# Kernel optimization log

Measured on AMD Instinct MI355X. Metric: run time of the kernel, lower is better.

Reference implementation:

```python
import jax, jax.numpy as jnp
import numpy as np

N = 100000   # num_nodes
D = 64       # input_dim
H = 128      # 2 * input_dim
E = 1_600_000
EPS = 1e-5   # BatchNorm1d eps


def setup_inputs() -> dict:
    key = jax.random.key(0)
    ks = jax.random.split(key, 8)
    # Embedding: xavier_normal_, padding_idx=0 row zeroed
    emb = jax.random.normal(ks[0], (N, D), jnp.float32) * np.float32(np.sqrt(2.0 / (N + D)))
    emb = emb.at[0].set(0.0)
    # GCNConv weights (glorot-ish scaling)
    W1 = jax.random.normal(ks[1], (D, H), jnp.float32) * np.float32(np.sqrt(2.0 / (D + H)))
    b1 = jnp.zeros((H,), jnp.float32)
    W2 = jax.random.normal(ks[2], (H, D), jnp.float32) * np.float32(np.sqrt(2.0 / (H + D)))
    b2 = jnp.zeros((D,), jnp.float32)
    gamma = jnp.ones((D,), jnp.float32)
    beta = jnp.zeros((D,), jnp.float32)
    edge_index = jax.random.randint(ks[3], (2, E), 0, N, dtype=jnp.int64)
    return {"emb": emb, "W1": W1, "b1": b1, "W2": W2, "b2": b2,
            "gamma": gamma, "beta": beta, "edge_index": edge_index}


def reference(emb, W1, b1, W2, b2, gamma, beta, edge_index):
    # --- gcn_norm: add self-loops, symmetric normalization (PyG default) ---
    self_loops = jnp.arange(N, dtype=edge_index.dtype)
    row = jnp.concatenate([edge_index[0], self_loops])  # source j
    col = jnp.concatenate([edge_index[1], self_loops])  # target i
    deg = jax.ops.segment_sum(jnp.ones(row.shape[0], emb.dtype), col, num_segments=N)
    deg_inv_sqrt = jnp.where(deg > 0, jax.lax.rsqrt(jnp.maximum(deg, 1.0)), 0.0)
    norm = deg_inv_sqrt[row] * deg_inv_sqrt[col]  # [E+N]

    def gcn_conv(x, W, b):
        h = x @ W                                  # linear first (PyG GCNConv)
        msg = h[row] * norm[:, None]               # gather + normalize
        out = jax.ops.segment_sum(msg, col, num_segments=N)  # scatter-aggregate
        return out + b

    h = gcn_conv(emb, W1, b1)   # [N, H]
    # dropout: identity in eval mode (deterministic reference)
    h = gcn_conv(h, W2, b2)     # [N, D]

    # BatchNorm1d, training-mode batch statistics (biased variance)
    mean = h.mean(axis=0)
    var = h.var(axis=0)
    return (h - mean) * jax.lax.rsqrt(var + EPS) * gamma + beta
```

## Files before the change

### kernel.cpp

```cpp
#include <hip/hip_runtime.h>


#define EPS_BN 1e-5f
#define NBKT_PAD 1024
#define BN_NB 128
#define SCAT_B 256

typedef _Float16 f16;
typedef _Float16 f16x2 __attribute__((ext_vector_type(2)));
typedef _Float16 f16x8 __attribute__((ext_vector_type(8)));
typedef float f32x4 __attribute__((ext_vector_type(4)));
union pk4 { ushort4 u; f16 h[4]; f16x2 h2[2]; };

__global__ __launch_bounds__(1024) void hist_k(const int* __restrict__ colv, int E, int epb,
                                               int* __restrict__ ghist) {
    __shared__ int bins[NBKT_PAD];
    int tid = threadIdx.x;
    bins[tid] = 0;
    __syncthreads();
    int e0 = blockIdx.x * epb;
    int e1 = min(E, e0 + epb);
    for (int e = e0 + tid; e < e1; e += 1024)
        atomicAdd(&bins[colv[e] >> 7], 1);
    __syncthreads();
    ghist[blockIdx.x * NBKT_PAD + tid] = bins[tid];
}

__global__ __launch_bounds__(256) void scan_bucket_k(int* __restrict__ ghist, int* __restrict__ bcnt) {
    __shared__ int s[256];
    int k = blockIdx.x;
    int b = threadIdx.x;
    int v = ghist[b * NBKT_PAD + k];
    s[b] = v; __syncthreads();
    for (int off = 1; off < 256; off <<= 1) {
        int t = (b >= off) ? s[b - off] : 0;
        __syncthreads();
        s[b] += t;
        __syncthreads();
    }
    ghist[b * NBKT_PAD + k] = s[b] - v;
    if (b == 255) bcnt[k] = s[255];
}

__global__ __launch_bounds__(1024) void scan_total_k(const int* __restrict__ bcnt,
                                                     int* __restrict__ bstart,
                                                     int* __restrict__ start, int n, int E) {
    __shared__ int s[1024];
    int tid = threadIdx.x;
    int v = bcnt[tid];
    s[tid] = v; __syncthreads();
    for (int off = 1; off < 1024; off <<= 1) {
        int t = (tid >= off) ? s[tid - off] : 0;
        __syncthreads();
        s[tid] += t;
        __syncthreads();
    }
    bstart[tid] = s[tid] - v;
    if (tid == 1023) bstart[1024] = s[1023];
    if (tid == 0) start[n] = E;
}

__global__ __launch_bounds__(1024) void scatB_k(const int* __restrict__ rowv, const int* __restrict__ colv,
                                                int E, int epb, const int* __restrict__ ghist,
                                                const int* __restrict__ bstart,
                                                unsigned* __restrict__ ebuf) {
    __shared__ int bins[NBKT_PAD];
    int tid = threadIdx.x;
    bins[tid] = ghist[blockIdx.x * NBKT_PAD + tid] + bstart[tid];
    __syncthreads();
    int e0 = blockIdx.x * epb;
    int e1 = min(E, e0 + epb);
    for (int e = e0 + tid; e < e1; e += 1024) {
        int c = colv[e];
        int p = atomicAdd(&bins[c >> 7], 1);
        ebuf[p] = ((unsigned)rowv[e] << 7) | (unsigned)(c & 127);
    }
}

__global__ __launch_bounds__(512) void buildC_k(const unsigned* __restrict__ ebuf,
                                                const int* __restrict__ bstart,
                                                int* __restrict__ start, int* __restrict__ srcs,
                                                float* __restrict__ dis, int n) {
    __shared__ int ncnt[128], noff[128], stmp[128];
    int b = blockIdx.x;
    int tid = threadIdx.x;
    int e0 = bstart[b], e1 = bstart[b + 1];
    if (tid < 128) ncnt[tid] = 0;
    __syncthreads();
    for (int e = e0 + tid; e < e1; e += 512)
        atomicAdd(&ncnt[ebuf[e] & 127u], 1);
    __syncthreads();
    if (tid < 128) stmp[tid] = ncnt[tid];
    __syncthreads();
    for (int off = 1; off < 128; off <<= 1) {
        int t = (tid < 128 && tid >= off) ? stmp[tid - off] : 0;
        __syncthreads();
        if (tid < 128) stmp[tid] += t;
        __syncthreads();
    }
    if (tid < 128) {
        int excl = stmp[tid] - ncnt[tid];
        noff[tid] = e0 + excl;
        int node = b * 128 + tid;
        if (node < n) {
            start[node] = e0 + excl;
            dis[node] = rsqrtf((float)(ncnt[tid] + 1));
        }
    }
    __syncthreads();
    for (int e = e0 + tid; e < e1; e += 512) {
        unsigned p = ebuf[e];
        int pos = atomicAdd(&noff[p & 127u], 1);
        srcs[pos] = (int)(p >> 7);
    }
}

__global__ __launch_bounds__(256) void wprep_k(const float* __restrict__ W1, const float* __restrict__ W2,
                                               f16* __restrict__ w1t, f16* __restrict__ w2t) {
    int t = blockIdx.x * 256 + threadIdx.x;
    if (t < 8192) {
        int k = t >> 7, c = t & 127;
        w1t[c * 64 + k] = (f16)W1[t];
    } else if (t < 16384) {
        int i = t - 8192;
        int k = i >> 6, c = i & 63;
        w2t[c * 128 + k] = (f16)W2[i];
    }
}

__global__ __launch_bounds__(256) void prescale_k(const float* __restrict__ emb,
                                                  const float* __restrict__ dis,
                                                  f16* __restrict__ es, int n) {
    int gid = blockIdx.x * 256 + threadIdx.x;
    int node = gid >> 4, q = gid & 15;
    if (node >= n) return;
    float d = dis[node];
    float4 v = ((const float4*)emb)[(size_t)node * 16 + q];
    pk4 p;
    p.h[0] = (f16)(v.x * d); p.h[1] = (f16)(v.y * d);
    p.h[2] = (f16)(v.z * d); p.h[3] = (f16)(v.w * d);
    ((ushort4*)es)[(size_t)node * 16 + q] = p.u;
}

__device__ __forceinline__ void acc_pk(float4& acc, ushort4 u) {
    pk4 p; p.u = u;
    acc.x += (float)p.h[0]; acc.y += (float)p.h[1];
    acc.z += (float)p.h[2]; acc.w += (float)p.h[3];
}

__global__ __launch_bounds__(256) void agg64_k(const f16* __restrict__ table, const int* __restrict__ start,
                                               const int* __restrict__ srcs, const float* __restrict__ dis,
                                               const float* __restrict__ bias, f16* __restrict__ out, int n) {
    int node = blockIdx.x * 16 + (threadIdx.x >> 4);
    if (node >= n) return;
    int lane = threadIdx.x & 15;
    const ushort4* t4 = (const ushort4*)table;
    float4 acc = make_float4(0.f, 0.f, 0.f, 0.f);
    acc_pk(acc, t4[(size_t)node * 16 + lane]);
    int s0 = start[node], s1 = start[node + 1];
    int e = s0;
    for (; e + 7 < s1; e += 8) {
        int i0 = srcs[e],     i1 = srcs[e + 1], i2 = srcs[e + 2], i3 = srcs[e + 3];
        int i4 = srcs[e + 4], i5 = srcs[e + 5], i6 = srcs[e + 6], i7 = srcs[e + 7];
        ushort4 v0 = t4[(size_t)i0 * 16 + lane];
        ushort4 v1 = t4[(size_t)i1 * 16 + lane];
        ushort4 v2 = t4[(size_t)i2 * 16 + lane];
        ushort4 v3 = t4[(size_t)i3 * 16 + lane];
        ushort4 v4 = t4[(size_t)i4 * 16 + lane];
        ushort4 v5 = t4[(size_t)i5 * 16 + lane];
        ushort4 v6 = t4[(size_t)i6 * 16 + lane];
        ushort4 v7 = t4[(size_t)i7 * 16 + lane];
        acc_pk(acc, v0); acc_pk(acc, v1); acc_pk(acc, v2); acc_pk(acc, v3);
        acc_pk(acc, v4); acc_pk(acc, v5); acc_pk(acc, v6); acc_pk(acc, v7);
    }
    for (; e + 3 < s1; e += 4) {
        int i0 = srcs[e], i1 = srcs[e + 1], i2 = srcs[e + 2], i3 = srcs[e + 3];
        ushort4 v0 = t4[(size_t)i0 * 16 + lane];
        ushort4 v1 = t4[(size_t)i1 * 16 + lane];
        ushort4 v2 = t4[(size_t)i2 * 16 + lane];
        ushort4 v3 = t4[(size_t)i3 * 16 + lane];
        acc_pk(acc, v0); acc_pk(acc, v1); acc_pk(acc, v2); acc_pk(acc, v3);
    }
    for (; e < s1; e++) acc_pk(acc, t4[(size_t)srcs[e] * 16 + lane]);
    float d = dis[node];
    float4 b = make_float4(0.f, 0.f, 0.f, 0.f);
    if (bias) b = ((const float4*)bias)[lane];
    pk4 p;
    p.h[0] = (f16)(acc.x * d + b.x); p.h[1] = (f16)(acc.y * d + b.y);
    p.h[2] = (f16)(acc.z * d + b.z); p.h[3] = (f16)(acc.w * d + b.w);
    ((ushort4*)out)[(size_t)node * 16 + lane] = p.u;
}

#define SH_PAD 136
__global__ __launch_bounds__(256) void gemmAB_mfma_k(const f16* __restrict__ ag1,
                                                     const f16* __restrict__ w1t,
                                                     const float* __restrict__ b1,
                                                     const f16* __restrict__ w2t,
                                                     const float* __restrict__ dis,
                                                     f16* __restrict__ hs2, int n) {
    __shared__ f16 sH[64 * SH_PAD];
    int tid = threadIdx.x;
    int w = tid >> 6, l = tid & 63;
    int cl = l & 15, ko = (l >> 4) * 8, r0 = (l >> 4) * 4;
    int rowbase = blockIdx.x * 64;
    int mrow = rowbase + w * 16;

    f16x8 a0 = *(const f16x8*)(ag1 + (size_t)(mrow + cl) * 64 + ko);
    f16x8 a1 = *(const f16x8*)(ag1 + (size_t)(mrow + cl) * 64 + 32 + ko);
#pragma unroll
    for (int nt = 0; nt < 8; nt++) {
        f32x4 acc = {0.f, 0.f, 0.f, 0.f};
        f16x8 b0 = *(const f16x8*)(w1t + (nt * 16 + cl) * 64 + ko);
        f16x8 b1f = *(const f16x8*)(w1t + (nt * 16 + cl) * 64 + 32 + ko);
        acc = __builtin_amdgcn_mfma_f32_16x16x32_f16(a0, b0, acc, 0, 0, 0);
        acc = __builtin_amdgcn_mfma_f32_16x16x32_f16(a1, b1f, acc, 0, 0, 0);
        float bias = b1[nt * 16 + cl];
#pragma unroll
        for (int j = 0; j < 4; j++)
            sH[(w * 16 + r0 + j) * SH_PAD + nt * 16 + cl] = (f16)(acc[j] + bias);
    }
    __syncthreads();
#pragma unroll
    for (int nt = 0; nt < 4; nt++) {
        f32x4 acc = {0.f, 0.f, 0.f, 0.f};
#pragma unroll
        for (int s = 0; s < 4; s++) {
            f16x8 a = *(const f16x8*)(&sH[(w * 16 + cl) * SH_PAD + s * 32 + ko]);
            f16x8 b = *(const f16x8*)(w2t + (nt * 16 + cl) * 128 + s * 32 + ko);
            acc = __builtin_amdgcn_mfma_f32_16x16x32_f16(a, b, acc, 0, 0, 0);
        }
#pragma unroll
        for (int j = 0; j < 4; j++) {
            int row = mrow + r0 + j;
            if (row < n) {
                float d = dis[row];
                hs2[(size_t)row * 64 + nt * 16 + cl] = (f16)(acc[j] * d);
            }
        }
    }
}

__global__ __launch_bounds__(256) void bn_part_k(const f16* __restrict__ x, float* __restrict__ pbuf, int n) {
    __shared__ float4 ls[256], lq[256];
    int q = threadIdx.x & 15;
    int rg = threadIdx.x >> 4;
    float4 s = make_float4(0.f, 0.f, 0.f, 0.f);
    float4 ss = make_float4(0.f, 0.f, 0.f, 0.f);
    for (int row = blockIdx.x * 16 + rg; row < n; row += gridDim.x * 16) {
        pk4 p; p.u = ((const ushort4*)x)[(size_t)row * 16 + q];
        float v0 = p.h[0], v1 = p.h[1], v2 = p.h[2], v3 = p.h[3];
        s.x += v0; s.y += v1; s.z += v2; s.w += v3;
        ss.x += v0 * v0; ss.y += v1 * v1; ss.z += v2 * v2; ss.w += v3 * v3;
    }
    ls[threadIdx.x] = s; lq[threadIdx.x] = ss;
    __syncthreads();
    if (threadIdx.x < 16) {
        float4 S = make_float4(0.f, 0.f, 0.f, 0.f);
        float4 Q = make_float4(0.f, 0.f, 0.f, 0.f);
        for (int g = 0; g < 16; g++) {
            float4 a = ls[g * 16 + threadIdx.x], b = lq[g * 16 + threadIdx.x];
            S.x += a.x; S.y += a.y; S.z += a.z; S.w += a.w;
            Q.x += b.x; Q.y += b.y; Q.z += b.z; Q.w += b.w;
        }
        float4* dst = (float4*)(pbuf + (size_t)blockIdx.x * 128);
        dst[threadIdx.x] = S;
        dst[threadIdx.x + 16] = Q;
    }
}

__global__ __launch_bounds__(64) void bn_final_k(const float* __restrict__ pbuf,
                                                 const float* __restrict__ gamma, const float* __restrict__ beta,
                                                 int n, float* __restrict__ scale, float* __restrict__ shift) {
    int c = threadIdx.x;
    float s = 0.f, q = 0.f;
    for (int b = 0; b < BN_NB; b++) {
        s += pbuf[b * 128 + c];
        q += pbuf[b * 128 + 64 + c];
    }
    float inv_n = 1.f / (float)n;
    float mean = s * inv_n;
    float var = q * inv_n - mean * mean;
    float sc = gamma[c] * rsqrtf(var + EPS_BN);
    scale[c] = sc;
    shift[c] = beta[c] - mean * sc;
}

__global__ __launch_bounds__(256) void bn_apply_k(const f16* __restrict__ x, const float* __restrict__ scale,
                                                  const float* __restrict__ shift, float* __restrict__ out, int n) {
    __shared__ float sscale[64], sshift[64];
    if (threadIdx.x < 64) {
        sscale[threadIdx.x] = scale[threadIdx.x];
        sshift[threadIdx.x] = shift[threadIdx.x];
    }
    __syncthreads();
    int i = blockIdx.x * 256 + threadIdx.x;
    if (i < n * 16) {
        int c = (i & 15) * 4;
        pk4 p; p.u = ((const ushort4*)x)[i];
        float4 o;
        o.x = (float)p.h[0] * sscale[c]     + sshift[c];
        o.y = (float)p.h[1] * sscale[c + 1] + sshift[c + 1];
        o.z = (float)p.h[2] * sscale[c + 2] + sshift[c + 2];
        o.w = (float)p.h[3] * sscale[c + 3] + sshift[c + 3];
        ((float4*)out)[i] = o;
    }
}

extern "C" void kernel_launch(void* const* d_in, const int* in_sizes, int n_in,
                              void* d_out, int out_size, void* d_ws, size_t ws_size,
                              hipStream_t stream) {
    const float* emb   = (const float*)d_in[0];
    const float* W1    = (const float*)d_in[1];
    const float* b1    = (const float*)d_in[2];
    const float* W2    = (const float*)d_in[3];
    const float* b2    = (const float*)d_in[4];
    const float* gamma = (const float*)d_in[5];
    const float* beta  = (const float*)d_in[6];
    const int*   ei    = (const int*)d_in[7];
    const int n = in_sizes[0] / 64;
    const int E = in_sizes[7] / 2;
    const int* rowv = ei;
    const int* colv = ei + E;
    const int NBKT = (n + 127) / 128;

    char* ws = (char*)d_ws;
    size_t o = 0;
    auto alloc = [&](size_t bytes) -> char* {
        char* p = ws + o;
        o = (o + bytes + 255) & ~(size_t)255;
        return p;
    };
    int*   ghist   = (int*)alloc((size_t)SCAT_B * NBKT_PAD * 4);
    int*   bcnt    = (int*)alloc(NBKT_PAD * 4);
    int*   bstart  = (int*)alloc((NBKT_PAD + 1) * 4);
    int*   start   = (int*)alloc((size_t)(n + 1) * 4);
    float* dis     = (float*)alloc((size_t)n * 4);
    int*   srcs    = (int*)alloc((size_t)E * 4);
    float* pbuf    = (float*)alloc(BN_NB * 128 * 4);
    float* bnscale = (float*)alloc(256);
    float* bnshift = (float*)alloc(256);
    f16*   w1t     = (f16*)alloc(128 * 64 * 2);
    f16*   w2t     = (f16*)alloc(64 * 128 * 2);
    f16*   es      = (f16*)alloc((size_t)n * 64 * 2);
    f16*   ag1     = (f16*)alloc((size_t)n * 64 * 2);
    f16*   hs2     = (f16*)alloc((size_t)n * 64 * 2);
    f16*   h2      = (f16*)alloc((size_t)n * 64 * 2);
    unsigned* ebuf = (unsigned*)alloc((size_t)E * 4);

    int epb = (E + SCAT_B - 1) / SCAT_B;

    hist_k<<<SCAT_B, 1024, 0, stream>>>(colv, E, epb, ghist);
    scan_bucket_k<<<NBKT_PAD, 256, 0, stream>>>(ghist, bcnt);
    scan_total_k<<<1, 1024, 0, stream>>>(bcnt, bstart, start, n, E);
    scatB_k<<<SCAT_B, 1024, 0, stream>>>(rowv, colv, E, epb, ghist, bstart, ebuf);
    buildC_k<<<NBKT, 512, 0, stream>>>(ebuf, bstart, start, srcs, dis, n);

    wprep_k<<<64, 256, 0, stream>>>(W1, W2, w1t, w2t);
    prescale_k<<<(n * 16 + 255) / 256, 256, 0, stream>>>(emb, dis, es, n);
    agg64_k<<<(n + 15) / 16, 256, 0, stream>>>(es, start, srcs, dis, nullptr, ag1, n);
    gemmAB_mfma_k<<<(n + 63) / 64, 256, 0, stream>>>(ag1, w1t, b1, w2t, dis, hs2, n);
    agg64_k<<<(n + 15) / 16, 256, 0, stream>>>(hs2, start, srcs, dis, b2, h2, n);

    bn_part_k<<<BN_NB, 256, 0, stream>>>(h2, pbuf, n);
    bn_final_k<<<1, 64, 0, stream>>>(pbuf, gamma, beta, n, bnscale, bnshift);
    bn_apply_k<<<(n * 16 + 255) / 256, 256, 0, stream>>>(h2, bnscale, bnshift, (float*)d_out, n);
}
```

Baseline: 179.8 us.

## Fuse weight prep, prescale, and BN partial stats into neighbouring kernels

Weight transposition moves into block 0 of the histogram kernel, embedding prescaling moves into buildC using the degree scales held in shared memory, and the BatchNorm partial sums are computed in the epilogue of the second aggregation. This removes three kernel launches and one full re-read of h2. In exchange, the final BN reduction must now sum about 6250 per-block partials instead of 128, so it is widened to 1024 threads. The aggregation kernel also gains a block barrier and extra shared memory.

```diff
diff --git a/kernel.cpp b/kernel.cpp
--- a/kernel.cpp
+++ b/kernel.cpp
@@ -3,7 +3,6 @@
 
 #define EPS_BN 1e-5f
 #define NBKT_PAD 1024
-#define BN_NB 128
 #define SCAT_B 256
 
 typedef _Float16 f16;
@@ -13,7 +12,9 @@
 union pk4 { ushort4 u; f16 h[4]; f16x2 h2[2]; };
 
 __global__ __launch_bounds__(1024) void hist_k(const int* __restrict__ colv, int E, int epb,
-                                               int* __restrict__ ghist) {
+                                               int* __restrict__ ghist,
+                                               const float* __restrict__ W1, const float* __restrict__ W2,
+                                               f16* __restrict__ w1t, f16* __restrict__ w2t) {
     __shared__ int bins[NBKT_PAD];
     int tid = threadIdx.x;
     bins[tid] = 0;
@@ -24,6 +25,18 @@
         atomicAdd(&bins[colv[e] >> 7], 1);
     __syncthreads();
     ghist[blockIdx.x * NBKT_PAD + tid] = bins[tid];
+    if (blockIdx.x == 0) {
+        for (int t = tid; t < 16384; t += 1024) {
+            if (t < 8192) {
+                int k = t >> 7, c = t & 127;
+                w1t[c * 64 + k] = (f16)W1[t];
+            } else {
+                int i = t - 8192;
+                int k = i >> 6, c = i & 63;
+                w2t[c * 128 + k] = (f16)W2[i];
+            }
+        }
+    }
 }
 
 __global__ __launch_bounds__(256) void scan_bucket_k(int* __restrict__ ghist, int* __restrict__ bcnt) {
@@ -80,8 +93,10 @@
 __global__ __launch_bounds__(512) void buildC_k(const unsigned* __restrict__ ebuf,
                                                 const int* __restrict__ bstart,
                                                 int* __restrict__ start, int* __restrict__ srcs,
-                                                float* __restrict__ dis, int n) {
+                                                float* __restrict__ dis,
+                                                const float* __restrict__ emb, f16* __restrict__ es, int n) {
     __shared__ int ncnt[128], noff[128], stmp[128];
+    __shared__ float sdis[128];
     int b = blockIdx.x;
     int tid = threadIdx.x;
     int e0 = bstart[b], e1 = bstart[b + 1];
@@ -101,10 +116,12 @@
     if (tid < 128) {
         int excl = stmp[tid] - ncnt[tid];
         noff[tid] = e0 + excl;
+        float d = rsqrtf((float)(ncnt[tid] + 1));
+        sdis[tid] = d;
         int node = b * 128 + tid;
         if (node < n) {
             start[node] = e0 + excl;
-            dis[node] = rsqrtf((float)(ncnt[tid] + 1));
+            dis[node] = d;
         }
     }
     __syncthreads();
@@ -113,33 +130,18 @@
         int pos = atomicAdd(&noff[p & 127u], 1);
         srcs[pos] = (int)(p >> 7);
     }
-}
-
-__global__ __launch_bounds__(256) void wprep_k(const float* __restrict__ W1, const float* __restrict__ W2,
-                                               f16* __restrict__ w1t, f16* __restrict__ w2t) {
-    int t = blockIdx.x * 256 + threadIdx.x;
-    if (t < 8192) {
-        int k = t >> 7, c = t & 127;
-        w1t[c * 64 + k] = (f16)W1[t];
-    } else if (t < 16384) {
-        int i = t - 8192;
-        int k = i >> 6, c = i & 63;
-        w2t[c * 128 + k] = (f16)W2[i];
-    }
-}
-
-__global__ __launch_bounds__(256) void prescale_k(const float* __restrict__ emb,
-                                                  const float* __restrict__ dis,
-                                                  f16* __restrict__ es, int n) {
-    int gid = blockIdx.x * 256 + threadIdx.x;
-    int node = gid >> 4, q = gid & 15;
-    if (node >= n) return;
-    float d = dis[node];
-    float4 v = ((const float4*)emb)[(size_t)node * 16 + q];
-    pk4 p;
-    p.h[0] = (f16)(v.x * d); p.h[1] = (f16)(v.y * d);
-    p.h[2] = (f16)(v.z * d); p.h[3] = (f16)(v.w * d);
-    ((ushort4*)es)[(size_t)node * 16 + q] = p.u;
+    for (int i = tid; i < 2048; i += 512) {
+        int r = i >> 4, q = i & 15;
+        int node = b * 128 + r;
+        if (node < n) {
+            float d = sdis[r];
+            float4 v = ((const float4*)emb)[(size_t)node * 16 + q];
+            pk4 p;
+            p.h[0] = (f16)(v.x * d); p.h[1] = (f16)(v.y * d);
+            p.h[2] = (f16)(v.z * d); p.h[3] = (f16)(v.w * d);
+            ((ushort4*)es)[(size_t)node * 16 + q] = p.u;
+        }
+    }
 }
 
 __device__ __forceinline__ void acc_pk(float4& acc, ushort4 u) {
@@ -150,14 +152,19 @@
 
 __global__ __launch_bounds__(256) void agg64_k(const f16* __restrict__ table, const int* __restrict__ start,
                                                const int* __restrict__ srcs, const float* __restrict__ dis,
-                                               const float* __restrict__ bias, f16* __restrict__ out, int n) {
+                                               const float* __restrict__ bias, f16* __restrict__ out,
+                                               float* __restrict__ pbuf, int n) {
+    __shared__ float4 ls[256], lq[256];
     int node = blockIdx.x * 16 + (threadIdx.x >> 4);
-    if (node >= n) return;
+    bool active = node < n;
     int lane = threadIdx.x & 15;
     const ushort4* t4 = (const ushort4*)table;
     float4 acc = make_float4(0.f, 0.f, 0.f, 0.f);
-    acc_pk(acc, t4[(size_t)node * 16 + lane]);
-    int s0 = start[node], s1 = start[node + 1];
+    int s0 = 0, s1 = 0;
+    if (active) {
+        acc_pk(acc, t4[(size_t)node * 16 + lane]);
+        s0 = start[node]; s1 = start[node + 1];
+    }
     int e = s0;
     for (; e + 7 < s1; e += 8) {
         int i0 = srcs[e],     i1 = srcs[e + 1], i2 = srcs[e + 2], i3 = srcs[e + 3];
@@ -182,13 +189,35 @@
         acc_pk(acc, v0); acc_pk(acc, v1); acc_pk(acc, v2); acc_pk(acc, v3);
     }
     for (; e < s1; e++) acc_pk(acc, t4[(size_t)srcs[e] * 16 + lane]);
-    float d = dis[node];
-    float4 b = make_float4(0.f, 0.f, 0.f, 0.f);
-    if (bias) b = ((const float4*)bias)[lane];
-    pk4 p;
-    p.h[0] = (f16)(acc.x * d + b.x); p.h[1] = (f16)(acc.y * d + b.y);
-    p.h[2] = (f16)(acc.z * d + b.z); p.h[3] = (f16)(acc.w * d + b.w);
-    ((ushort4*)out)[(size_t)node * 16 + lane] = p.u;
+    float4 o = make_float4(0.f, 0.f, 0.f, 0.f);
+    if (active) {
+        float d = dis[node];
+        float4 b = make_float4(0.f, 0.f, 0.f, 0.f);
+        if (bias) b = ((const float4*)bias)[lane];
+        o.x = acc.x * d + b.x; o.y = acc.y * d + b.y;
+        o.z = acc.z * d + b.z; o.w = acc.w * d + b.w;
+        pk4 p;
+        p.h[0] = (f16)o.x; p.h[1] = (f16)o.y; p.h[2] = (f16)o.z; p.h[3] = (f16)o.w;
+        ((ushort4*)out)[(size_t)node * 16 + lane] = p.u;
+    }
+    if (pbuf) {
+        float4 sq;
+        sq.x = o.x * o.x; sq.y = o.y * o.y; sq.z = o.z * o.z; sq.w = o.w * o.w;
+        ls[threadIdx.x] = o; lq[threadIdx.x] = sq;
+        __syncthreads();
+        if (threadIdx.x < 16) {
+            float4 S = make_float4(0.f, 0.f, 0.f, 0.f);
+            float4 Q = make_float4(0.f, 0.f, 0.f, 0.f);
+            for (int g = 0; g < 16; g++) {
+                float4 a = ls[g * 16 + threadIdx.x], c = lq[g * 16 + threadIdx.x];
+                S.x += a.x; S.y += a.y; S.z += a.z; S.w += a.w;
+                Q.x += c.x; Q.y += c.y; Q.z += c.z; Q.w += c.w;
+            }
+            float4* dst = (float4*)(pbuf + (size_t)blockIdx.x * 128);
+            dst[threadIdx.x] = S;
+            dst[threadIdx.x + 16] = Q;
+        }
+    }
 }
 
 #define SH_PAD 136
@@ -240,49 +269,33 @@
     }
 }
 
-__global__ __launch_bounds__(256) void bn_part_k(const f16* __restrict__ x, float* __restrict__ pbuf, int n) {
-    __shared__ float4 ls[256], lq[256];
-    int q = threadIdx.x & 15;
-    int rg = threadIdx.x >> 4;
-    float4 s = make_float4(0.f, 0.f, 0.f, 0.f);
-    float4 ss = make_float4(0.f, 0.f, 0.f, 0.f);
-    for (int row = blockIdx.x * 16 + rg; row < n; row += gridDim.x * 16) {
-        pk4 p; p.u = ((const ushort4*)x)[(size_t)row * 16 + q];
-        float v0 = p.h[0], v1 = p.h[1], v2 = p.h[2], v3 = p.h[3];
-        s.x += v0; s.y += v1; s.z += v2; s.w += v3;
-        ss.x += v0 * v0; ss.y += v1 * v1; ss.z += v2 * v2; ss.w += v3 * v3;
-    }
-    ls[threadIdx.x] = s; lq[threadIdx.x] = ss;
-    __syncthreads();
-    if (threadIdx.x < 16) {
-        float4 S = make_float4(0.f, 0.f, 0.f, 0.f);
-        float4 Q = make_float4(0.f, 0.f, 0.f, 0.f);
-        for (int g = 0; g < 16; g++) {
-            float4 a = ls[g * 16 + threadIdx.x], b = lq[g * 16 + threadIdx.x];
-            S.x += a.x; S.y += a.y; S.z += a.z; S.w += a.w;
-            Q.x += b.x; Q.y += b.y; Q.z += b.z; Q.w += b.w;
-        }
-        float4* dst = (float4*)(pbuf + (size_t)blockIdx.x * 128);
-        dst[threadIdx.x] = S;
-        dst[threadIdx.x + 16] = Q;
-    }
-}
-
-__global__ __launch_bounds__(64) void bn_final_k(const float* __restrict__ pbuf,
-                                                 const float* __restrict__ gamma, const float* __restrict__ beta,
-                                                 int n, float* __restrict__ scale, float* __restrict__ shift) {
-    int c = threadIdx.x;
+__global__ __launch_bounds__(1024) void bn_final_k(const float* __restrict__ pbuf,
+                                                   const float* __restrict__ gamma,
+                                                   const float* __restrict__ beta,
+                                                   int n, int nb,
+                                                   float* __restrict__ scale, float* __restrict__ shift) {
+    __shared__ float ls[1024], lq[1024];
+    int c = threadIdx.x & 63, part = threadIdx.x >> 6;
     float s = 0.f, q = 0.f;
-    for (int b = 0; b < BN_NB; b++) {
-        s += pbuf[b * 128 + c];
-        q += pbuf[b * 128 + 64 + c];
-    }
-    float inv_n = 1.f / (float)n;
-    float mean = s * inv_n;
-    float var = q * inv_n - mean * mean;
-    float sc = gamma[c] * rsqrtf(var + EPS_BN);
-    scale[c] = sc;
-    shift[c] = beta[c] - mean * sc;
+    for (int b = part; b < nb; b += 16) {
+        s += pbuf[(size_t)b * 128 + c];
+        q += pbuf[(size_t)b * 128 + 64 + c];
+    }
+    ls[threadIdx.x] = s; lq[threadIdx.x] = q;
+    __syncthreads();
+    if (threadIdx.x < 64) {
+        s = 0.f; q = 0.f;
+        for (int k = 0; k < 16; k++) {
+            s += ls[k * 64 + c];
+            q += lq[k * 64 + c];
+        }
+        float inv_n = 1.f / (float)n;
+        float mean = s * inv_n;
+        float var = q * inv_n - mean * mean;
+        float sc = gamma[c] * rsqrtf(var + EPS_BN);
+        scale[c] = sc;
+        shift[c] = beta[c] - mean * sc;
+    }
 }
 
 __global__ __launch_bounds__(256) void bn_apply_k(const f16* __restrict__ x, const float* __restrict__ scale,
@@ -322,6 +335,7 @@
     const int* rowv = ei;
     const int* colv = ei + E;
     const int NBKT = (n + 127) / 128;
+    const int NAGG = (n + 15) / 16;
 
     char* ws = (char*)d_ws;
     size_t o = 0;
@@ -336,7 +350,7 @@
     int*   start   = (int*)alloc((size_t)(n + 1) * 4);
     float* dis     = (float*)alloc((size_t)n * 4);
     int*   srcs    = (int*)alloc((size_t)E * 4);
-    float* pbuf    = (float*)alloc(BN_NB * 128 * 4);
+    float* pbuf    = (float*)alloc((size_t)NAGG * 128 * 4);
     float* bnscale = (float*)alloc(256);
     float* bnshift = (float*)alloc(256);
     f16*   w1t     = (f16*)alloc(128 * 64 * 2);
@@ -349,19 +363,16 @@
 
     int epb = (E + SCAT_B - 1) / SCAT_B;
 
-    hist_k<<<SCAT_B, 1024, 0, stream>>>(colv, E, epb, ghist);
+    hist_k<<<SCAT_B, 1024, 0, stream>>>(colv, E, epb, ghist, W1, W2, w1t, w2t);
     scan_bucket_k<<<NBKT_PAD, 256, 0, stream>>>(ghist, bcnt);
     scan_total_k<<<1, 1024, 0, stream>>>(bcnt, bstart, start, n, E);
     scatB_k<<<SCAT_B, 1024, 0, stream>>>(rowv, colv, E, epb, ghist, bstart, ebuf);
-    buildC_k<<<NBKT, 512, 0, stream>>>(ebuf, bstart, start, srcs, dis, n);
-
-    wprep_k<<<64, 256, 0, stream>>>(W1, W2, w1t, w2t);
-    prescale_k<<<(n * 16 + 255) / 256, 256, 0, stream>>>(emb, dis, es, n);
-    agg64_k<<<(n + 15) / 16, 256, 0, stream>>>(es, start, srcs, dis, nullptr, ag1, n);
+    buildC_k<<<NBKT, 512, 0, stream>>>(ebuf, bstart, start, srcs, dis, emb, es, n);
+
+    agg64_k<<<NAGG, 256, 0, stream>>>(es, start, srcs, dis, nullptr, ag1, nullptr, n);
     gemmAB_mfma_k<<<(n + 63) / 64, 256, 0, stream>>>(ag1, w1t, b1, w2t, dis, hs2, n);
-    agg64_k<<<(n + 15) / 16, 256, 0, stream>>>(hs2, start, srcs, dis, b2, h2, n);
-
-    bn_part_k<<<BN_NB, 256, 0, stream>>>(h2, pbuf, n);
-    bn_final_k<<<1, 64, 0, stream>>>(pbuf, gamma, beta, n, bnscale, bnshift);
+    agg64_k<<<NAGG, 256, 0, stream>>>(hs2, start, srcs, dis, b2, h2, pbuf, n);
+
+    bn_final_k<<<1, 1024, 0, stream>>>(pbuf, gamma, beta, n, NAGG, bnscale, bnshift);
     bn_apply_k<<<(n * 16 + 255) / 256, 256, 0, stream>>>(h2, bnscale, bnshift, (float*)d_out, n);
 }
```

Result: slower. 278.9 us (+55.1%).
